# Kernel optimization log

Measured on AMD Instinct MI355X. Metric: run time of the kernel, lower is better.

## Reference

```python
import jax, jax.numpy as jnp
import numpy as np

N_FINE, N_COARSE, E_POOL, E_PP, C = 100000, 25000, 100000, 400000, 128

def setup_inputs() -> dict:
    key = jax.random.key(0)
    ks = jax.random.split(key, 24)
    d = {}
    d['x'] = jax.random.normal(ks[0], (N_FINE, C), jnp.float32)
    d['pool_src'] = jax.random.randint(ks[1], (E_POOL,), 0, N_FINE)
    d['pool_dst'] = jax.random.randint(ks[2], (E_POOL,), 0, N_COARSE)
    d['pool_attr'] = jax.random.uniform(ks[3], (E_POOL,), jnp.float32)
    d['pp_src'] = jax.random.randint(ks[4], (E_PP,), 0, N_COARSE)
    d['pp_dst'] = jax.random.randint(ks[5], (E_PP,), 0, N_COARSE)
    d['pp_attr'] = jax.random.uniform(ks[6], (E_PP,), jnp.float32)
    d['unpool_src'] = jax.random.randint(ks[7], (E_POOL,), 0, N_COARSE)
    d['unpool_dst'] = jax.random.randint(ks[8], (E_POOL,), 0, N_FINE)
    d['unpool_attr'] = jax.random.uniform(ks[9], (E_POOL,), jnp.float32)
    s = 1.0 / np.sqrt(C)
    for i in range(4):
        d[f'w{i+1}_self'] = jax.random.normal(ks[10 + 3 * i], (C, C), jnp.float32) * s
        d[f'w{i+1}_neigh'] = jax.random.normal(ks[11 + 3 * i], (C, C), jnp.float32) * s
        d[f'b{i+1}'] = jnp.zeros((C,), jnp.float32)
    d['n_coarse'] = N_COARSE
    d['n_fine'] = N_FINE
    return d

def reference(x, pool_src, pool_dst, pool_attr, pp_src, pp_dst, pp_attr,
              unpool_src, unpool_dst, unpool_attr,
              w1_self, w1_neigh, b1, w2_self, w2_neigh, b2,
              w3_self, w3_neigh, b3, w4_self, w4_neigh, b4,
              n_coarse, n_fine):
    # Pooling: edge-weighted scatter-add from fine nodes to coarse nodes.
    h = jax.ops.segment_sum(pool_attr[:, None] * x[pool_src], pool_dst,
                            num_segments=n_coarse)  # [n_coarse, C]
    def conv(h, ws, wn, b):
        # Message passing: gather src features, scale by edge_attr, scatter to dst.
        agg = jax.ops.segment_sum(pp_attr[:, None] * h[pp_src], pp_dst,
                                  num_segments=n_coarse)
        return jax.nn.relu(h @ ws + agg @ wn + b)
    h = conv(h, w1_self, w1_neigh, b1)
    h = conv(h, w2_self, w2_neigh, b2)
    h = conv(h, w3_self, w3_neigh, b3)
    h = conv(h, w4_self, w4_neigh, b4)
    # Unpooling: edge-weighted scatter-add from coarse back to fine nodes.
    out = jax.ops.segment_sum(unpool_attr[:, None] * h[unpool_src], unpool_dst,
                              num_segments=n_fine)  # [n_fine, C]
    return out
```

## Files before the change

kernel.cpp:

```cpp
#include <hip/hip_runtime.h>
#include <hip/hip_bf16.h>

#define C 128
#define NC 25000
#define CAP_PL 32
#define CAP_PP 64
#define CAP_UP 16

typedef __attribute__((ext_vector_type(8))) short bf16x8;
typedef __attribute__((ext_vector_type(4))) float f32x4;

static __device__ __forceinline__ unsigned short f2bf(float x) {
    __hip_bfloat16 h = __float2bfloat16(x);
    return __builtin_bit_cast(unsigned short, h);
}
static __device__ __forceinline__ float bflo(unsigned int v) {
    return __builtin_bit_cast(float, v << 16);
}
static __device__ __forceinline__ float bfhi(unsigned int v) {
    return __builtin_bit_cast(float, v & 0xffff0000u);
}

__global__ __launch_bounds__(256) void prep_k(
    const float* __restrict__ w0s, const float* __restrict__ w0n,
    const float* __restrict__ w1s, const float* __restrict__ w1n,
    const float* __restrict__ w2s, const float* __restrict__ w2n,
    const float* __restrict__ w3s, const float* __restrict__ w3n,
    unsigned short* __restrict__ wt, int* __restrict__ cnt, int tot) {
    int b = blockIdx.x;
    if (b < 512) {
        int i = b * 256 + threadIdx.x;
        int l = i >> 15;
        int r = i & 32767;
        int col = r >> 8, k = r & 255;
        const float* ws = (l == 0) ? w0s : (l == 1) ? w1s : (l == 2) ? w2s : w3s;
        const float* wn = (l == 0) ? w0n : (l == 1) ? w1n : (l == 2) ? w2n : w3n;
        float v = (k < 128) ? ws[k * 128 + col] : wn[(k - 128) * 128 + col];
        wt[i] = f2bf(v);
    } else {
        int i = (b - 512) * 256 + threadIdx.x;
        if (i < tot) cnt[i] = 0;
    }
}

__global__ __launch_bounds__(256) void fill_direct_k(
    const int* __restrict__ pl_src, const int* __restrict__ pl_dst, const float* __restrict__ pl_attr,
    const int* __restrict__ pp_src, const int* __restrict__ pp_dst, const float* __restrict__ pp_attr,
    const int* __restrict__ up_src, const int* __restrict__ up_dst, const float* __restrict__ up_attr,
    int* __restrict__ cnt, int2* __restrict__ ep_pl, int2* __restrict__ ep_pp,
    int2* __restrict__ ep_up, int Epl, int Epp, int Eup) {
    int i = blockIdx.x * blockDim.x + threadIdx.x;
    if (i < Epl) {
        int d = pl_dst[i];
        int p = atomicAdd(&cnt[d], 1);
        if (p < CAP_PL) ep_pl[d * CAP_PL + p] = make_int2(pl_src[i], __float_as_int(pl_attr[i]));
    } else if (i < Epl + Epp) {
        int j = i - Epl;
        int d = pp_dst[j];
        int p = atomicAdd(&cnt[NC + d], 1);
        if (p < CAP_PP) ep_pp[d * CAP_PP + p] = make_int2(pp_src[j], __float_as_int(pp_attr[j]));
    } else if (i < Epl + Epp + Eup) {
        int j = i - Epl - Epp;
        int d = up_dst[j];
        int p = atomicAdd(&cnt[2 * NC + d], 1);
        if (p < CAP_UP) ep_up[d * CAP_UP + p] = make_int2(up_src[j], __float_as_int(up_attr[j]));
    }
}

template<int CAP, bool IN_BF16, bool OUT_BF16>
__global__ __launch_bounds__(256) void gather_k(
    const void* __restrict__ in_, const int* __restrict__ cnt,
    const int2* __restrict__ ep, void* __restrict__ out_, int n) {
    int node = (blockIdx.x * 256 + threadIdx.x) >> 4;
    if (node >= n) return;
    int lane = threadIdx.x & 15;
    int deg = cnt[node];
    deg = deg < CAP ? deg : CAP;
    int e0 = node * CAP, e1 = e0 + deg;
    float acc[8];
#pragma unroll
    for (int j = 0; j < 8; ++j) acc[j] = 0.f;

    const unsigned int* inb = (const unsigned int*)in_;
    const float* inf = (const float*)in_;

    auto edge = [&](int s, int abits) {
        float a0 = __int_as_float(abits);
        if (IN_BF16) {
            uint4 v0 = *(const uint4*)(inb + (size_t)s * 64 + lane * 4);
            acc[0] = fmaf(a0, bflo(v0.x), acc[0]); acc[1] = fmaf(a0, bfhi(v0.x), acc[1]);
            acc[2] = fmaf(a0, bflo(v0.y), acc[2]); acc[3] = fmaf(a0, bfhi(v0.y), acc[3]);
            acc[4] = fmaf(a0, bflo(v0.z), acc[4]); acc[5] = fmaf(a0, bfhi(v0.z), acc[5]);
            acc[6] = fmaf(a0, bflo(v0.w), acc[6]); acc[7] = fmaf(a0, bfhi(v0.w), acc[7]);
        } else {
            const float* r0 = inf + (size_t)s * C + lane * 8;
            float4 u0 = *(const float4*)r0, u1 = *(const float4*)(r0 + 4);
            acc[0] = fmaf(a0, u0.x, acc[0]); acc[1] = fmaf(a0, u0.y, acc[1]);
            acc[2] = fmaf(a0, u0.z, acc[2]); acc[3] = fmaf(a0, u0.w, acc[3]);
            acc[4] = fmaf(a0, u1.x, acc[4]); acc[5] = fmaf(a0, u1.y, acc[5]);
            acc[6] = fmaf(a0, u1.z, acc[6]); acc[7] = fmaf(a0, u1.w, acc[7]);
        }
    };

    int e = e0;
    for (; e + 1 < e1; e += 2) {
        int4 pq = *(const int4*)(ep + e);
        edge(pq.x, pq.y);
        edge(pq.z, pq.w);
    }
    if (e < e1) {
        int2 p0 = ep[e];
        edge(p0.x, p0.y);
    }

    if (OUT_BF16) {
        uint4 r;
        r.x = (unsigned)f2bf(acc[0]) | ((unsigned)f2bf(acc[1]) << 16);
        r.y = (unsigned)f2bf(acc[2]) | ((unsigned)f2bf(acc[3]) << 16);
        r.z = (unsigned)f2bf(acc[4]) | ((unsigned)f2bf(acc[5]) << 16);
        r.w = (unsigned)f2bf(acc[6]) | ((unsigned)f2bf(acc[7]) << 16);
        *(uint4*)((unsigned int*)out_ + (size_t)node * 64 + lane * 4) = r;
    } else {
        f32x4* ob = (f32x4*)((float*)out_ + (size_t)node * C + lane * 8);
        f32x4 v0 = {acc[0], acc[1], acc[2], acc[3]};
        f32x4 v1 = {acc[4], acc[5], acc[6], acc[7]};
        __builtin_nontemporal_store(v0, ob);
        __builtin_nontemporal_store(v1, ob + 1);
    }
}

__global__ __launch_bounds__(256, 2) void conv_mfma_k(
    const unsigned short* __restrict__ hin, const unsigned short* __restrict__ agg,
    const unsigned short* __restrict__ wt, const float* __restrict__ bias,
    unsigned short* __restrict__ hout, int n) {
    const int wv = threadIdx.x >> 6;
    const int lane = threadIdx.x & 63;
    const int col0 = wv * 32;
    const int r0 = blockIdx.x * 64;
    if (r0 >= n) return;
    const int q = lane >> 4;
    const int lr = lane & 15;

    bf16x8 bfr[2][8];
#pragma unroll
    for (int nt = 0; nt < 2; ++nt) {
        int col = col0 + nt * 16 + lr;
#pragma unroll
        for (int kk = 0; kk < 8; ++kk)
            bfr[nt][kk] = *(const bf16x8*)(wt + col * 256 + kk * 32 + q * 8);
    }

    f32x4 acc[4][2];
#pragma unroll
    for (int m = 0; m < 4; ++m)
#pragma unroll
        for (int nt = 0; nt < 2; ++nt) acc[m][nt] = (f32x4)(0.f);

    int rowb[4];
#pragma unroll
    for (int m = 0; m < 4; ++m) {
        int row = r0 + m * 16 + lr;
        rowb[m] = (row < n) ? row : (n - 1);
    }

#pragma unroll
    for (int kk = 0; kk < 8; ++kk) {
        const unsigned short* srcbase = (kk < 4) ? hin : agg;
        const int koff = (kk & 3) * 32 + q * 8;
#pragma unroll
        for (int m = 0; m < 4; ++m) {
            bf16x8 a = *(const bf16x8*)(srcbase + (size_t)rowb[m] * C + koff);
#pragma unroll
            for (int nt = 0; nt < 2; ++nt)
                acc[m][nt] = __builtin_amdgcn_mfma_f32_16x16x32_bf16(
                    a, bfr[nt][kk], acc[m][nt], 0, 0, 0);
        }
    }

#pragma unroll
    for (int nt = 0; nt < 2; ++nt) {
        int col = col0 + nt * 16 + lr;
        float bv = bias[col];
#pragma unroll
        for (int m = 0; m < 4; ++m) {
#pragma unroll
            for (int r = 0; r < 4; ++r) {
                int row = r0 + m * 16 + q * 4 + r;
                if (row < n) {
                    float v = acc[m][nt][r] + bv;
                    hout[(size_t)row * C + col] = f2bf(v > 0.f ? v : 0.f);
                }
            }
        }
    }
}


extern "C" void kernel_launch(void* const* d_in, const int* in_sizes, int n_in,
                              void* d_out, int out_size, void* d_ws, size_t ws_size,
                              hipStream_t stream) {
    const float* x         = (const float*)d_in[0];
    const int*   pool_src  = (const int*)d_in[1];
    const int*   pool_dst  = (const int*)d_in[2];
    const float* pool_attr = (const float*)d_in[3];
    const int*   pp_src    = (const int*)d_in[4];
    const int*   pp_dst    = (const int*)d_in[5];
    const float* pp_attr   = (const float*)d_in[6];
    const int*   up_src    = (const int*)d_in[7];
    const int*   up_dst    = (const int*)d_in[8];
    const float* up_attr   = (const float*)d_in[9];
    const float* w[12];
    for (int i = 0; i < 12; ++i) w[i] = (const float*)d_in[10 + i];

    const int E_pool = in_sizes[1];
    const int E_pp   = in_sizes[4];
    const int E_up   = in_sizes[7];
    const int NF     = in_sizes[0] / C;
    const int TOT    = 2 * NC + NF;
    const int TE     = E_pool + E_pp + E_up;

    unsigned short* h   = (unsigned short*)d_ws;
    unsigned short* h2  = h + (size_t)NC * C;
    unsigned short* agg = h2 + (size_t)NC * C;
    int*  cnt_all = (int*)(agg + (size_t)NC * C);
    int2* ep_pl   = (int2*)(((size_t)(cnt_all + TOT) + 15) & ~(size_t)15);
    int2* ep_pp   = ep_pl + (size_t)NC * CAP_PL;
    int2* ep_up   = ep_pp + (size_t)NC * CAP_PP;
    unsigned short* wt = (unsigned short*)(ep_up + (size_t)NF * CAP_UP);

    const int* pl_cnt = cnt_all;
    const int* pp_cnt = cnt_all + NC;
    const int* up_cnt = cnt_all + 2 * NC;

    const int TB = 256;

    prep_k<<<512 + (TOT + TB - 1) / TB, TB, 0, stream>>>(
        w[0], w[1], w[3], w[4], w[6], w[7], w[9], w[10], wt, cnt_all, TOT);

    fill_direct_k<<<(TE + TB - 1) / TB, TB, 0, stream>>>(
        pool_src, pool_dst, pool_attr, pp_src, pp_dst, pp_attr,
        up_src, up_dst, up_attr, cnt_all, ep_pl, ep_pp, ep_up,
        E_pool, E_pp, E_up);

    gather_k<CAP_PL, false, true><<<((size_t)NC * 16 + 255) / 256, 256, 0, stream>>>(
        x, pl_cnt, ep_pl, h, NC);

    unsigned short* hcur = h;
    unsigned short* halt = h2;
    const int mtiles = (NC + 63) / 64;
    for (int l = 0; l < 4; ++l) {
        gather_k<CAP_PP, true, true><<<((size_t)NC * 16 + 255) / 256, 256, 0, stream>>>(
            hcur, pp_cnt, ep_pp, agg, NC);
        conv_mfma_k<<<mtiles, 256, 0, stream>>>(
            hcur, agg, wt + (size_t)l * 128 * 256, w[3 * l + 2], halt, NC);
        unsigned short* t = hcur; hcur = halt; halt = t;
    }

    gather_k<CAP_UP, true, false><<<((size_t)NF * 16 + 255) / 256, 256, 0, stream>>>(
        hcur, up_cnt, ep_up, (float*)d_out, NF);
}
```

Baseline: 201.9 us.

## Replace per-node global atomics with two-pass binned edge bucketing

Edge-list construction moves from a single pass with global atomics on per-destination counters to two passes. The first pass scatters each edge into one of 8 sub-bins per 256-node range, using far fewer atomic targets. The second pass gives each 256-node range to one block, which counts and places its edges with shared-memory atomics and writes the per-node counts once. This is meant to cut global atomic contention and scattered writes, at the cost of an extra kernel launch and an intermediate int4 buffer write and read. Edges are dropped if a sub-bin exceeds 768 entries.

```diff
diff --git a/kernel.cpp b/kernel.cpp
--- a/kernel.cpp
+++ b/kernel.cpp
@@ -6,6 +6,7 @@
 #define CAP_PL 32
 #define CAP_PP 64
 #define CAP_UP 16
+#define SBCAP 768
 
 typedef __attribute__((ext_vector_type(8))) short bf16x8;
 typedef __attribute__((ext_vector_type(4))) float f32x4;
@@ -26,7 +27,7 @@
     const float* __restrict__ w1s, const float* __restrict__ w1n,
     const float* __restrict__ w2s, const float* __restrict__ w2n,
     const float* __restrict__ w3s, const float* __restrict__ w3n,
-    unsigned short* __restrict__ wt, int* __restrict__ cnt, int tot) {
+    unsigned short* __restrict__ wt, int* __restrict__ bincnt, int nsub) {
     int b = blockIdx.x;
     if (b < 512) {
         int i = b * 256 + threadIdx.x;
@@ -39,32 +40,62 @@
         wt[i] = f2bf(v);
     } else {
         int i = (b - 512) * 256 + threadIdx.x;
-        if (i < tot) cnt[i] = 0;
-    }
-}
-
-__global__ __launch_bounds__(256) void fill_direct_k(
+        if (i < nsub) bincnt[i] = 0;
+    }
+}
+
+__global__ __launch_bounds__(256) void binA_k(
     const int* __restrict__ pl_src, const int* __restrict__ pl_dst, const float* __restrict__ pl_attr,
     const int* __restrict__ pp_src, const int* __restrict__ pp_dst, const float* __restrict__ pp_attr,
     const int* __restrict__ up_src, const int* __restrict__ up_dst, const float* __restrict__ up_attr,
-    int* __restrict__ cnt, int2* __restrict__ ep_pl, int2* __restrict__ ep_pp,
-    int2* __restrict__ ep_up, int Epl, int Epp, int Eup) {
+    int* __restrict__ bincnt, int4* __restrict__ bins, int Epl, int Epp, int Eup) {
     int i = blockIdx.x * blockDim.x + threadIdx.x;
+    int cidx, s; float a;
     if (i < Epl) {
-        int d = pl_dst[i];
-        int p = atomicAdd(&cnt[d], 1);
-        if (p < CAP_PL) ep_pl[d * CAP_PL + p] = make_int2(pl_src[i], __float_as_int(pl_attr[i]));
+        cidx = pl_dst[i]; s = pl_src[i]; a = pl_attr[i];
     } else if (i < Epl + Epp) {
         int j = i - Epl;
-        int d = pp_dst[j];
-        int p = atomicAdd(&cnt[NC + d], 1);
-        if (p < CAP_PP) ep_pp[d * CAP_PP + p] = make_int2(pp_src[j], __float_as_int(pp_attr[j]));
+        cidx = NC + pp_dst[j]; s = pp_src[j]; a = pp_attr[j];
     } else if (i < Epl + Epp + Eup) {
         int j = i - Epl - Epp;
-        int d = up_dst[j];
-        int p = atomicAdd(&cnt[2 * NC + d], 1);
-        if (p < CAP_UP) ep_up[d * CAP_UP + p] = make_int2(up_src[j], __float_as_int(up_attr[j]));
-    }
+        cidx = 2 * NC + up_dst[j]; s = up_src[j]; a = up_attr[j];
+    } else return;
+    int sub = (cidx >> 8) * 8 + (blockIdx.x & 7);
+    int p = atomicAdd(&bincnt[sub], 1);
+    if (p < SBCAP) bins[(size_t)sub * SBCAP + p] = make_int4(s, __float_as_int(a), cidx, 0);
+}
+
+__global__ __launch_bounds__(256) void binB_k(
+    const int* __restrict__ bincnt, const int4* __restrict__ bins,
+    int* __restrict__ cnt, int2* __restrict__ ep_pl, int2* __restrict__ ep_pp,
+    int2* __restrict__ ep_up, int tot) {
+    __shared__ int lcnt[256];
+    const int tid = threadIdx.x;
+    const int bin = blockIdx.x;
+    lcnt[tid] = 0;
+    __syncthreads();
+#pragma unroll 1
+    for (int g = 0; g < 8; ++g) {
+        int sub = bin * 8 + g;
+        int ne = bincnt[sub];
+        ne = ne < SBCAP ? ne : SBCAP;
+        const int4* bp = bins + (size_t)sub * SBCAP;
+        for (int i = tid; i < ne; i += 256) {
+            int4 e = bp[i];
+            int p = atomicAdd(&lcnt[e.z & 255], 1);
+            int cidx = e.z;
+            if (cidx < NC) {
+                if (p < CAP_PL) ep_pl[cidx * CAP_PL + p] = make_int2(e.x, e.y);
+            } else if (cidx < 2 * NC) {
+                if (p < CAP_PP) ep_pp[(cidx - NC) * CAP_PP + p] = make_int2(e.x, e.y);
+            } else {
+                if (p < CAP_UP) ep_up[(cidx - 2 * NC) * CAP_UP + p] = make_int2(e.x, e.y);
+            }
+        }
+    }
+    __syncthreads();
+    int node = (bin << 8) + tid;
+    if (node < tot) cnt[node] = lcnt[tid];
 }
 
 template<int CAP, bool IN_BF16, bool OUT_BF16>
@@ -218,15 +249,19 @@
     const int NF     = in_sizes[0] / C;
     const int TOT    = 2 * NC + NF;
     const int TE     = E_pool + E_pp + E_up;
+    const int NBINS  = (TOT + 255) >> 8;
+    const int NSUB   = NBINS * 8;
 
     unsigned short* h   = (unsigned short*)d_ws;
     unsigned short* h2  = h + (size_t)NC * C;
     unsigned short* agg = h2 + (size_t)NC * C;
     int*  cnt_all = (int*)(agg + (size_t)NC * C);
-    int2* ep_pl   = (int2*)(((size_t)(cnt_all + TOT) + 15) & ~(size_t)15);
+    int*  bincnt  = cnt_all + TOT;
+    int2* ep_pl   = (int2*)(((size_t)(bincnt + NSUB) + 15) & ~(size_t)15);
     int2* ep_pp   = ep_pl + (size_t)NC * CAP_PL;
     int2* ep_up   = ep_pp + (size_t)NC * CAP_PP;
-    unsigned short* wt = (unsigned short*)(ep_up + (size_t)NF * CAP_UP);
+    int4* bins    = (int4*)(ep_up + (size_t)NF * CAP_UP);
+    unsigned short* wt = (unsigned short*)(bins + (size_t)NSUB * SBCAP);
 
     const int* pl_cnt = cnt_all;
     const int* pp_cnt = cnt_all + NC;
@@ -234,13 +269,15 @@
 
     const int TB = 256;
 
-    prep_k<<<512 + (TOT + TB - 1) / TB, TB, 0, stream>>>(
-        w[0], w[1], w[3], w[4], w[6], w[7], w[9], w[10], wt, cnt_all, TOT);
-
-    fill_direct_k<<<(TE + TB - 1) / TB, TB, 0, stream>>>(
+    prep_k<<<512 + (NSUB + TB - 1) / TB, TB, 0, stream>>>(
+        w[0], w[1], w[3], w[4], w[6], w[7], w[9], w[10], wt, bincnt, NSUB);
+
+    binA_k<<<(TE + TB - 1) / TB, TB, 0, stream>>>(
         pool_src, pool_dst, pool_attr, pp_src, pp_dst, pp_attr,
-        up_src, up_dst, up_attr, cnt_all, ep_pl, ep_pp, ep_up,
-        E_pool, E_pp, E_up);
+        up_src, up_dst, up_attr, bincnt, bins, E_pool, E_pp, E_up);
+
+    binB_k<<<NBINS, TB, 0, stream>>>(
+        bincnt, bins, cnt_all, ep_pl, ep_pp, ep_up, TOT);
 
     gather_k<CAP_PL, false, true><<<((size_t)NC * 16 + 255) / 256, 256, 0, stream>>>(
         x, pl_cnt, ep_pl, h, NC);
```

Measured after the change: 327.5 us. 1.62x slower.

## Fuse message-passing gather into MFMA conv kernel via shared-memory aggregate tile

Applied to the files above, without the earlier changes.

Each conv layer now runs one kernel instead of two. Every block of 16 coarse nodes first gathers and edge-weights its neighbour features into a swizzled LDS tile, then runs the bf16 MFMA self/neighbour matmul straight from that tile. This drops the separate gather launch and the global write and re-read of the agg buffer. In exchange, each block now reloads the full weight fragment for only 16 rows (it previously covered 64). The gather and the matmul phases of a block are also serialized by a barrier.

```diff
diff --git a/kernel.cpp b/kernel.cpp
--- a/kernel.cpp
+++ b/kernel.cpp
@@ -129,17 +129,18 @@
     }
 }
 
-__global__ __launch_bounds__(256, 2) void conv_mfma_k(
-    const unsigned short* __restrict__ hin, const unsigned short* __restrict__ agg,
-    const unsigned short* __restrict__ wt, const float* __restrict__ bias,
-    unsigned short* __restrict__ hout, int n) {
-    const int wv = threadIdx.x >> 6;
-    const int lane = threadIdx.x & 63;
-    const int col0 = wv * 32;
-    const int r0 = blockIdx.x * 64;
-    if (r0 >= n) return;
+__global__ __launch_bounds__(256, 4) void gconv16_k(
+    const unsigned short* __restrict__ hin, const int* __restrict__ cnt,
+    const int2* __restrict__ ep, const unsigned short* __restrict__ wt,
+    const float* __restrict__ bias, unsigned short* __restrict__ hout, int n) {
+    __shared__ unsigned int aggs[16 * 64];
+    const int tid = threadIdx.x;
+    const int r0 = blockIdx.x * 16;
+    const int wv = tid >> 6;
+    const int lane = tid & 63;
     const int q = lane >> 4;
     const int lr = lane & 15;
+    const int col0 = wv * 32;
 
     bf16x8 bfr[2][8];
 #pragma unroll
@@ -150,31 +151,71 @@
             bfr[nt][kk] = *(const bf16x8*)(wt + col * 256 + kk * 32 + q * 8);
     }
 
-    f32x4 acc[4][2];
-#pragma unroll
-    for (int m = 0; m < 4; ++m)
-#pragma unroll
-        for (int nt = 0; nt < 2; ++nt) acc[m][nt] = (f32x4)(0.f);
-
-    int rowb[4];
-#pragma unroll
-    for (int m = 0; m < 4; ++m) {
-        int row = r0 + m * 16 + lr;
-        rowb[m] = (row < n) ? row : (n - 1);
-    }
+    {
+        const int qw = tid >> 4, l16 = tid & 15;
+        const unsigned int* inb = (const unsigned int*)hin;
+        int node = r0 + qw;
+        float acc[8];
+#pragma unroll
+        for (int j = 0; j < 8; ++j) acc[j] = 0.f;
+        if (node < n) {
+            int deg = cnt[node];
+            deg = deg < CAP_PP ? deg : CAP_PP;
+            int e = node * CAP_PP, e1 = e + deg;
+            for (; e + 1 < e1; e += 2) {
+                int4 pq = *(const int4*)(ep + e);
+                float a0 = __int_as_float(pq.y), a1 = __int_as_float(pq.w);
+                uint4 v0 = *(const uint4*)(inb + (size_t)pq.x * 64 + l16 * 4);
+                uint4 v1 = *(const uint4*)(inb + (size_t)pq.z * 64 + l16 * 4);
+                acc[0] = fmaf(a0, bflo(v0.x), acc[0]); acc[1] = fmaf(a0, bfhi(v0.x), acc[1]);
+                acc[2] = fmaf(a0, bflo(v0.y), acc[2]); acc[3] = fmaf(a0, bfhi(v0.y), acc[3]);
+                acc[4] = fmaf(a0, bflo(v0.z), acc[4]); acc[5] = fmaf(a0, bfhi(v0.z), acc[5]);
+                acc[6] = fmaf(a0, bflo(v0.w), acc[6]); acc[7] = fmaf(a0, bfhi(v0.w), acc[7]);
+                acc[0] = fmaf(a1, bflo(v1.x), acc[0]); acc[1] = fmaf(a1, bfhi(v1.x), acc[1]);
+                acc[2] = fmaf(a1, bflo(v1.y), acc[2]); acc[3] = fmaf(a1, bfhi(v1.y), acc[3]);
+                acc[4] = fmaf(a1, bflo(v1.z), acc[4]); acc[5] = fmaf(a1, bfhi(v1.z), acc[5]);
+                acc[6] = fmaf(a1, bflo(v1.w), acc[6]); acc[7] = fmaf(a1, bfhi(v1.w), acc[7]);
+            }
+            if (e < e1) {
+                int2 p0 = ep[e];
+                float a0 = __int_as_float(p0.y);
+                uint4 v0 = *(const uint4*)(inb + (size_t)p0.x * 64 + l16 * 4);
+                acc[0] = fmaf(a0, bflo(v0.x), acc[0]); acc[1] = fmaf(a0, bfhi(v0.x), acc[1]);
+                acc[2] = fmaf(a0, bflo(v0.y), acc[2]); acc[3] = fmaf(a0, bfhi(v0.y), acc[3]);
+                acc[4] = fmaf(a0, bflo(v0.z), acc[4]); acc[5] = fmaf(a0, bfhi(v0.z), acc[5]);
+                acc[6] = fmaf(a0, bflo(v0.w), acc[6]); acc[7] = fmaf(a0, bfhi(v0.w), acc[7]);
+            }
+        }
+        uint4 r;
+        r.x = (unsigned)f2bf(acc[0]) | ((unsigned)f2bf(acc[1]) << 16);
+        r.y = (unsigned)f2bf(acc[2]) | ((unsigned)f2bf(acc[3]) << 16);
+        r.z = (unsigned)f2bf(acc[4]) | ((unsigned)f2bf(acc[5]) << 16);
+        r.w = (unsigned)f2bf(acc[6]) | ((unsigned)f2bf(acc[7]) << 16);
+        *(uint4*)(aggs + qw * 64 + ((l16 ^ qw) << 2)) = r;
+    }
+    __syncthreads();
+
+    if (r0 >= n) return;
+    f32x4 acc2[2];
+    acc2[0] = (f32x4)(0.f);
+    acc2[1] = (f32x4)(0.f);
+
+    int rowa = r0 + lr;
+    if (rowa >= n) rowa = n - 1;
 
 #pragma unroll
     for (int kk = 0; kk < 8; ++kk) {
-        const unsigned short* srcbase = (kk < 4) ? hin : agg;
-        const int koff = (kk & 3) * 32 + q * 8;
-#pragma unroll
-        for (int m = 0; m < 4; ++m) {
-            bf16x8 a = *(const bf16x8*)(srcbase + (size_t)rowb[m] * C + koff);
-#pragma unroll
-            for (int nt = 0; nt < 2; ++nt)
-                acc[m][nt] = __builtin_amdgcn_mfma_f32_16x16x32_bf16(
-                    a, bfr[nt][kk], acc[m][nt], 0, 0, 0);
-        }
+        bf16x8 a;
+        if (kk < 4) {
+            a = *(const bf16x8*)(hin + (size_t)rowa * C + kk * 32 + q * 8);
+        } else {
+            int g = ((kk - 4) * 4 + q) ^ lr;
+            a = *(const bf16x8*)(aggs + lr * 64 + g * 4);
+        }
+#pragma unroll
+        for (int nt = 0; nt < 2; ++nt)
+            acc2[nt] = __builtin_amdgcn_mfma_f32_16x16x32_bf16(
+                a, bfr[nt][kk], acc2[nt], 0, 0, 0);
     }
 
 #pragma unroll
@@ -182,14 +223,11 @@
         int col = col0 + nt * 16 + lr;
         float bv = bias[col];
 #pragma unroll
-        for (int m = 0; m < 4; ++m) {
-#pragma unroll
-            for (int r = 0; r < 4; ++r) {
-                int row = r0 + m * 16 + q * 4 + r;
-                if (row < n) {
-                    float v = acc[m][nt][r] + bv;
-                    hout[(size_t)row * C + col] = f2bf(v > 0.f ? v : 0.f);
-                }
+        for (int r = 0; r < 4; ++r) {
+            int row = r0 + q * 4 + r;
+            if (row < n) {
+                float v = acc2[nt][r] + bv;
+                hout[(size_t)row * C + col] = f2bf(v > 0.f ? v : 0.f);
             }
         }
     }
@@ -221,8 +259,7 @@
 
     unsigned short* h   = (unsigned short*)d_ws;
     unsigned short* h2  = h + (size_t)NC * C;
-    unsigned short* agg = h2 + (size_t)NC * C;
-    int*  cnt_all = (int*)(agg + (size_t)NC * C);
+    int*  cnt_all = (int*)(h2 + (size_t)NC * C);
     int2* ep_pl   = (int2*)(((size_t)(cnt_all + TOT) + 15) & ~(size_t)15);
     int2* ep_pp   = ep_pl + (size_t)NC * CAP_PL;
     int2* ep_up   = ep_pp + (size_t)NC * CAP_PP;
@@ -247,12 +284,10 @@
 
     unsigned short* hcur = h;
     unsigned short* halt = h2;
-    const int mtiles = (NC + 63) / 64;
+    const int gtiles = (NC + 15) / 16;
     for (int l = 0; l < 4; ++l) {
-        gather_k<CAP_PP, true, true><<<((size_t)NC * 16 + 255) / 256, 256, 0, stream>>>(
-            hcur, pp_cnt, ep_pp, agg, NC);
-        conv_mfma_k<<<mtiles, 256, 0, stream>>>(
-            hcur, agg, wt + (size_t)l * 128 * 256, w[3 * l + 2], halt, NC);
+        gconv16_k<<<gtiles, 256, 0, stream>>>(
+            hcur, pp_cnt, ep_pp, wt + (size_t)l * 128 * 256, w[3 * l + 2], halt, NC);
         unsigned short* t = hcur; hcur = halt; halt = t;
     }
 
```

Result: slower. 220.9 us (+9.4%).
